# Performance work log

Hardware: AMD Instinct MI355X
Metric: run time of the kernel (lower is better)

The kernel has to match this reference:

```python
import jax, jax.numpy as jnp
import numpy as np

N_USERS, N_ITEMS, D, B = 16384, 4096, 64, 2048
NAN_FRAC = 0.7
EPS = 1e-8


def setup_inputs() -> dict:
    key = jax.random.key(0)
    k1, k2, k3, k4, k5 = jax.random.split(key, 5)
    ratings = jax.random.uniform(k1, (N_USERS, N_ITEMS), jnp.float32, 1.0, 5.0)
    miss = jax.random.uniform(k2, (N_USERS, N_ITEMS)) < NAN_FRAC
    rating_matrix = jnp.where(miss, jnp.nan, ratings)
    user_embeddings = jax.random.normal(k3, (N_USERS, D), jnp.float32)
    user_indices = jax.random.randint(k4, (B,), 0, N_USERS)
    item_indices = jax.random.randint(k5, (B,), 0, N_ITEMS)
    return {
        "rating_matrix": rating_matrix,
        "user_embeddings": user_embeddings,
        "user_indices": user_indices,
        "item_indices": item_indices,
    }


def reference(rating_matrix, user_embeddings, user_indices, item_indices):
    n_users = rating_matrix.shape[0]

    # per-user average over non-NaN ratings (0.0 if user has no ratings)
    valid_r = ~jnp.isnan(rating_matrix)                      # [N, I]
    r0 = jnp.where(valid_r, rating_matrix, 0.0)
    cnt = valid_r.sum(axis=1)
    avg_ratings = jnp.where(cnt > 0, r0.sum(axis=1) / jnp.maximum(cnt, 1), 0.0)  # [N]

    u = user_embeddings[user_indices]                        # [B, d]
    # cosine similarity of each query user vs all users
    dots = jnp.einsum('bd,nd->bn', u, user_embeddings)       # [B, N]
    mag_u = jnp.linalg.norm(u, axis=1, keepdims=True)        # [B, 1]
    mag_v = jnp.linalg.norm(user_embeddings, axis=1)[None]   # [1, N]
    sim = dots / (mag_u * mag_v + EPS)                       # [B, N]

    # ratings of all users on each query item
    ratings_col = rating_matrix[:, item_indices].T           # [B, N]
    mask = ~jnp.isnan(ratings_col)                           # valid neighbor ratings
    mask = mask & (jnp.arange(n_users)[None, :] != user_indices[:, None])  # exclude self

    diff = jnp.where(mask, ratings_col - avg_ratings[None, :], 0.0)
    sim_m = jnp.where(mask, sim, 0.0)
    num = (diff * sim_m).sum(axis=1)                         # [B]
    den = jnp.abs(sim_m).sum(axis=1)                         # [B]
    den_safe = jnp.where(den == 0, 1.0, den)

    avg_u = avg_ratings[user_indices]
    return jnp.where(den == 0, avg_u, avg_u + num / den_safe)
```

## Files before the change

kernel.cpp:

```cpp
#include <hip/hip_runtime.h>
#include <math.h>

#define NU   16384
#define NI   4096
#define DDIM 64
#define BB   2048

typedef unsigned short ushort_t;
typedef __attribute__((ext_vector_type(8))) short short8;
typedef __attribute__((ext_vector_type(4))) float f32x4;

static __device__ __forceinline__ unsigned short f2bf(float f) {
    union { float f; unsigned int u; } v; v.f = f;
    unsigned int u = v.u + 0x7FFFu + ((v.u >> 16) & 1u);
    return (unsigned short)(u >> 16);
}
static __device__ __forceinline__ float bf2f(unsigned short h) {
    union { unsigned int u; float f; } v; v.u = ((unsigned int)h) << 16;
    return v.f;
}

__global__ __launch_bounds__(256) void k_qprep(
    const float* __restrict__ E, const int* __restrict__ uidx,
    ushort_t* __restrict__ Ubf, int2* __restrict__ qinfo)
{
    const int lane = threadIdx.x & 63;
    const int b = blockIdx.x * 4 + (threadIdx.x >> 6);
    const int ub = uidx[b];
    const float e = E[(size_t)ub * DDIM + lane];
    float ss = e * e;
#pragma unroll
    for (int o = 32; o > 0; o >>= 1) ss += __shfl_xor(ss, o);
    Ubf[b * DDIM + lane] = f2bf(e);
    if (lane == 0) qinfo[b] = make_int2(ub, __float_as_int(rsqrtf(ss)));
}

__global__ __launch_bounds__(256) void k_rowgather(
    const float* __restrict__ R, const float* __restrict__ E,
    const int* __restrict__ iidx,
    float2* __restrict__ ani, ushort_t* __restrict__ Gbf)
{
    __shared__ ushort_t rowb[4][NI];
    __shared__ ushort_t s_ii[BB];
    const int tid  = threadIdx.x;
    const int lane = tid & 63;
    const int wid  = tid >> 6;

    for (int t = tid; t < BB; t += 256) s_ii[t] = (ushort_t)iidx[t];
    __syncthreads();

    const int gw = blockIdx.x * 4 + wid;
#pragma unroll 1
    for (int rr = 0; rr < 4; ++rr) {
        const int n = gw * 4 + rr;
        const float4* R4 = (const float4*)(R + (size_t)n * NI);
        float sum = 0.f, cnt = 0.f;
#pragma unroll
        for (int g = 0; g < 4; ++g) {
            float4 vv[4];
#pragma unroll
            for (int j = 0; j < 4; ++j) vv[j] = R4[(g * 4 + j) * 64 + lane];
#pragma unroll
            for (int j = 0; j < 4; ++j) {
                const float4 v = vv[j];
                if (v.x == v.x) { sum += v.x; cnt += 1.f; }
                if (v.y == v.y) { sum += v.y; cnt += 1.f; }
                if (v.z == v.z) { sum += v.z; cnt += 1.f; }
                if (v.w == v.w) { sum += v.w; cnt += 1.f; }
                ushort4 h;
                h.x = f2bf(v.x); h.y = f2bf(v.y); h.z = f2bf(v.z); h.w = f2bf(v.w);
                *(ushort4*)&rowb[wid][((g * 4 + j) * 64 + lane) * 4] = h;
            }
        }
        const float e = E[(size_t)n * DDIM + lane];
        float ss = e * e;
#pragma unroll
        for (int o = 32; o > 0; o >>= 1) ss += __shfl_xor(ss, o);
#pragma unroll
        for (int o = 32; o > 0; o >>= 1) {
            sum += __shfl_xor(sum, o);
            cnt += __shfl_xor(cnt, o);
        }
        if (lane == 0) {
            const float avg = (cnt > 0.f) ? (sum / cnt) : 0.f;
            ani[n] = make_float2(avg, rsqrtf(ss));
        }
        asm volatile("s_waitcnt lgkmcnt(0)" ::: "memory");
        ushort_t* Gn = Gbf + (size_t)n * BB;
#pragma unroll
        for (int it = 0; it < 32; ++it) {
            const int b = it * 64 + lane;
            Gn[b] = rowb[wid][s_ii[b]];
        }
    }
}

__global__ __launch_bounds__(256) void k_accum(
    const float* __restrict__ E, const ushort_t* __restrict__ Ubf,
    const ushort_t* __restrict__ Gbf, const float2* __restrict__ ani,
    const int2* __restrict__ qinfo, float2* __restrict__ partials)
{
    const int tid  = threadIdx.x;
    const int lane = tid & 63;
    const int w    = tid >> 6;
    const int lo   = lane & 15;
    const int hi   = lane >> 4;
    const int n0   = blockIdx.x * 16;

    short8 a[2];
#pragma unroll
    for (int kg = 0; kg < 2; ++kg) {
        const float* ep = E + (size_t)(n0 + lo) * DDIM + kg * 32 + hi * 8;
        const float4 e0 = *(const float4*)(ep);
        const float4 e1 = *(const float4*)(ep + 4);
        union { short8 v; ushort_t u[8]; } t;
        t.u[0] = f2bf(e0.x); t.u[1] = f2bf(e0.y); t.u[2] = f2bf(e0.z); t.u[3] = f2bf(e0.w);
        t.u[4] = f2bf(e1.x); t.u[5] = f2bf(e1.y); t.u[6] = f2bf(e1.z); t.u[7] = f2bf(e1.w);
        a[kg] = t.v;
    }
    float2 anir[4];
#pragma unroll
    for (int r = 0; r < 4; ++r) anir[r] = ani[n0 + hi * 4 + r];

    float2* pout = partials + (size_t)blockIdx.x * BB;

#pragma unroll 1
    for (int j = 0; j < 32; ++j) {
        const int b0 = (j * 4 + w) * 16;
        const int2 q = qinfo[b0 + lo];
        const float inv_mu = __int_as_float(q.y);

        short8 bf[2];
#pragma unroll
        for (int kg = 0; kg < 2; ++kg)
            bf[kg] = *(const short8*)(Ubf + (size_t)(b0 + lo) * DDIM + kg * 32 + hi * 8);

        f32x4 c = {0.f, 0.f, 0.f, 0.f};
        c = __builtin_amdgcn_mfma_f32_16x16x32_bf16(a[0], bf[0], c, 0, 0, 0);
        c = __builtin_amdgcn_mfma_f32_16x16x32_bf16(a[1], bf[1], c, 0, 0, 0);

        float fnum = 0.f, fden = 0.f;
#pragma unroll
        for (int r = 0; r < 4; ++r) {
            const int nr = n0 + hi * 4 + r;
            const float g = bf2f(Gbf[(size_t)nr * BB + b0 + lo]);
            const bool valid = (g == g) && (nr != q.x);
            const float s  = valid ? c[r] * (inv_mu * anir[r].y) : 0.f;
            const float gv = valid ? g : 0.f;
            fnum += (gv - anir[r].x) * s;
            fden += fabsf(s);
        }
        fnum += __shfl_xor(fnum, 16); fden += __shfl_xor(fden, 16);
        fnum += __shfl_xor(fnum, 32); fden += __shfl_xor(fden, 32);
        if (lane < 16) pout[b0 + lane] = make_float2(fnum, fden);
    }
}

__global__ __launch_bounds__(256) void k_final(
    const float2* __restrict__ partials, const float2* __restrict__ ani,
    const int2* __restrict__ qinfo, float* __restrict__ out)
{
    __shared__ float sn[8][32], sd[8][32];
    const int tid = threadIdx.x;
    const int bl  = tid & 31;
    const int ch  = tid >> 5;
    const int b   = blockIdx.x * 32 + bl;
    float n = 0.f, d = 0.f;
    for (int blk = ch; blk < NU / 16; blk += 8) {
        const float2 p = partials[(size_t)blk * BB + b];
        n += p.x; d += p.y;
    }
    sn[ch][bl] = n; sd[ch][bl] = d;
    __syncthreads();
    if (tid < 32) {
        float N = 0.f, D = 0.f;
#pragma unroll
        for (int c2 = 0; c2 < 8; ++c2) { N += sn[c2][tid]; D += sd[c2][tid]; }
        const int bb = blockIdx.x * 32 + tid;
        const float au = ani[qinfo[bb].x].x;
        out[bb] = (D == 0.f) ? au : (au + N / D);
    }
}

extern "C" void kernel_launch(void* const* d_in, const int* in_sizes, int n_in,
                              void* d_out, int out_size, void* d_ws, size_t ws_size,
                              hipStream_t stream)
{
    const float* R    = (const float*)d_in[0];
    const float* E    = (const float*)d_in[1];
    const int*   uidx = (const int*)d_in[2];
    const int*   iidx = (const int*)d_in[3];
    float* out = (float*)d_out;

    char* p = (char*)d_ws;
    ushort_t* Gbf   = (ushort_t*)p;              p += (size_t)NU * BB * 2;
    float2*   parts = (float2*)p;                p += (size_t)(NU / 16) * BB * 8;
    ushort_t* Ubf   = (ushort_t*)p;              p += (size_t)BB * DDIM * 2;
    float2*   ani   = (float2*)p;                p += (size_t)NU * 8;
    int2*     qinfo = (int2*)p;                  p += (size_t)BB * 8;

    k_qprep<<<BB / 4, 256, 0, stream>>>(E, uidx, Ubf, qinfo);
    k_rowgather<<<NU / 16, 256, 0, stream>>>(R, E, iidx, ani, Gbf);
    k_accum<<<NU / 16, 256, 0, stream>>>(E, Ubf, Gbf, ani, qinfo, parts);
    k_final<<<BB / 32, 256, 0, stream>>>(parts, ani, qinfo, out);
}
```

Baseline: 463.2 us.

## Fuse row gather and accumulation to keep gathered ratings in shared memory

Merges the row-gather and accumulate kernels into one block-per-16-users kernel. Each block gathers the selected item columns for its 16 users into a padded shared tile instead of writing a 64 MB bf16 gather buffer to global memory and reading it back. This removes that global round-trip and one launch. In exchange, shared memory per block rises to about 74 KB, which lowers occupancy, and the row-loading loop now has two block barriers per row.

Measured after the change: 440.5 us. 1.05x faster.

```diff
diff --git a/kernel.cpp b/kernel.cpp
--- a/kernel.cpp
+++ b/kernel.cpp
@@ -5,24 +5,25 @@
 #define NI   4096
 #define DDIM 64
 #define BB   2048
-
-typedef unsigned short ushort_t;
+#define GSTR 2052
+
+typedef unsigned short u16;
 typedef __attribute__((ext_vector_type(8))) short short8;
 typedef __attribute__((ext_vector_type(4))) float f32x4;
 
-static __device__ __forceinline__ unsigned short f2bf(float f) {
+static __device__ __forceinline__ u16 f2bf(float f) {
     union { float f; unsigned int u; } v; v.f = f;
     unsigned int u = v.u + 0x7FFFu + ((v.u >> 16) & 1u);
-    return (unsigned short)(u >> 16);
-}
-static __device__ __forceinline__ float bf2f(unsigned short h) {
+    return (u16)(u >> 16);
+}
+static __device__ __forceinline__ float bf2f(u16 h) {
     union { unsigned int u; float f; } v; v.u = ((unsigned int)h) << 16;
     return v.f;
 }
 
 __global__ __launch_bounds__(256) void k_qprep(
     const float* __restrict__ E, const int* __restrict__ uidx,
-    ushort_t* __restrict__ Ubf, int2* __restrict__ qinfo)
+    u16* __restrict__ Ubf, int2* __restrict__ qinfo)
 {
     const int lane = threadIdx.x & 63;
     const int b = blockIdx.x * 4 + (threadIdx.x >> 6);
@@ -35,77 +36,82 @@
     if (lane == 0) qinfo[b] = make_int2(ub, __float_as_int(rsqrtf(ss)));
 }
 
-__global__ __launch_bounds__(256) void k_rowgather(
+__global__ __launch_bounds__(256) void k_fused(
     const float* __restrict__ R, const float* __restrict__ E,
-    const int* __restrict__ iidx,
-    float2* __restrict__ ani, ushort_t* __restrict__ Gbf)
-{
-    __shared__ ushort_t rowb[4][NI];
-    __shared__ ushort_t s_ii[BB];
+    const int* __restrict__ iidx, const u16* __restrict__ Ubf,
+    const int2* __restrict__ qinfo, float2* __restrict__ partials,
+    float* __restrict__ avgAll)
+{
+    __shared__ u16 s_ii[BB];
+    __shared__ u16 row[NI];
+    __shared__ u16 g[16][GSTR];
+    __shared__ float sAvg[16], sInv[16];
+    __shared__ float redS[4], redC[4];
+
     const int tid  = threadIdx.x;
     const int lane = tid & 63;
     const int wid  = tid >> 6;
-
-    for (int t = tid; t < BB; t += 256) s_ii[t] = (ushort_t)iidx[t];
-    __syncthreads();
-
-    const int gw = blockIdx.x * 4 + wid;
-#pragma unroll 1
-    for (int rr = 0; rr < 4; ++rr) {
-        const int n = gw * 4 + rr;
-        const float4* R4 = (const float4*)(R + (size_t)n * NI);
-        float sum = 0.f, cnt = 0.f;
-#pragma unroll
-        for (int g = 0; g < 4; ++g) {
-            float4 vv[4];
-#pragma unroll
-            for (int j = 0; j < 4; ++j) vv[j] = R4[(g * 4 + j) * 64 + lane];
-#pragma unroll
-            for (int j = 0; j < 4; ++j) {
-                const float4 v = vv[j];
-                if (v.x == v.x) { sum += v.x; cnt += 1.f; }
-                if (v.y == v.y) { sum += v.y; cnt += 1.f; }
-                if (v.z == v.z) { sum += v.z; cnt += 1.f; }
-                if (v.w == v.w) { sum += v.w; cnt += 1.f; }
-                ushort4 h;
-                h.x = f2bf(v.x); h.y = f2bf(v.y); h.z = f2bf(v.z); h.w = f2bf(v.w);
-                *(ushort4*)&rowb[wid][((g * 4 + j) * 64 + lane) * 4] = h;
-            }
-        }
+    const int n0   = blockIdx.x * 16;
+
+    for (int t = tid; t < BB; t += 256) s_ii[t] = (u16)iidx[t];
+
+#pragma unroll
+    for (int rs = 0; rs < 4; ++rs) {
+        const int n = n0 + wid * 4 + rs;
         const float e = E[(size_t)n * DDIM + lane];
         float ss = e * e;
 #pragma unroll
         for (int o = 32; o > 0; o >>= 1) ss += __shfl_xor(ss, o);
+        if (lane == 0) sInv[wid * 4 + rs] = rsqrtf(ss);
+    }
+
+#pragma unroll 1
+    for (int rr = 0; rr < 16; ++rr) {
+        const int n = n0 + rr;
+        const float4* R4 = (const float4*)(R + (size_t)n * NI);
+        float4 vv[4];
+#pragma unroll
+        for (int j = 0; j < 4; ++j) vv[j] = R4[tid + j * 256];
+
+        __syncthreads();
+
+        float sum = 0.f, cnt = 0.f;
+#pragma unroll
+        for (int j = 0; j < 4; ++j) {
+            const float4 v = vv[j];
+            if (v.x == v.x) { sum += v.x; cnt += 1.f; }
+            if (v.y == v.y) { sum += v.y; cnt += 1.f; }
+            if (v.z == v.z) { sum += v.z; cnt += 1.f; }
+            if (v.w == v.w) { sum += v.w; cnt += 1.f; }
+            ushort4 h;
+            h.x = f2bf(v.x); h.y = f2bf(v.y); h.z = f2bf(v.z); h.w = f2bf(v.w);
+            *(ushort4*)&row[(tid + j * 256) * 4] = h;
+        }
 #pragma unroll
         for (int o = 32; o > 0; o >>= 1) {
             sum += __shfl_xor(sum, o);
             cnt += __shfl_xor(cnt, o);
         }
-        if (lane == 0) {
-            const float avg = (cnt > 0.f) ? (sum / cnt) : 0.f;
-            ani[n] = make_float2(avg, rsqrtf(ss));
-        }
-        asm volatile("s_waitcnt lgkmcnt(0)" ::: "memory");
-        ushort_t* Gn = Gbf + (size_t)n * BB;
-#pragma unroll
-        for (int it = 0; it < 32; ++it) {
-            const int b = it * 64 + lane;
-            Gn[b] = rowb[wid][s_ii[b]];
-        }
-    }
-}
-
-__global__ __launch_bounds__(256) void k_accum(
-    const float* __restrict__ E, const ushort_t* __restrict__ Ubf,
-    const ushort_t* __restrict__ Gbf, const float2* __restrict__ ani,
-    const int2* __restrict__ qinfo, float2* __restrict__ partials)
-{
-    const int tid  = threadIdx.x;
-    const int lane = tid & 63;
-    const int w    = tid >> 6;
-    const int lo   = lane & 15;
-    const int hi   = lane >> 4;
-    const int n0   = blockIdx.x * 16;
+        if (lane == 0) { redS[wid] = sum; redC[wid] = cnt; }
+
+        __syncthreads();
+        if (tid == 0) {
+            const float S = redS[0] + redS[1] + redS[2] + redS[3];
+            const float C = redC[0] + redC[1] + redC[2] + redC[3];
+            const float a = (C > 0.f) ? (S / C) : 0.f;
+            sAvg[rr] = a;
+            avgAll[n] = a;
+        }
+#pragma unroll
+        for (int t = 0; t < 8; ++t) {
+            const int b = tid + t * 256;
+            g[rr][b] = row[s_ii[b]];
+        }
+    }
+    __syncthreads();
+
+    const int lo = lane & 15;
+    const int hi = lane >> 4;
 
     short8 a[2];
 #pragma unroll
@@ -113,41 +119,39 @@
         const float* ep = E + (size_t)(n0 + lo) * DDIM + kg * 32 + hi * 8;
         const float4 e0 = *(const float4*)(ep);
         const float4 e1 = *(const float4*)(ep + 4);
-        union { short8 v; ushort_t u[8]; } t;
+        union { short8 v; u16 u[8]; } t;
         t.u[0] = f2bf(e0.x); t.u[1] = f2bf(e0.y); t.u[2] = f2bf(e0.z); t.u[3] = f2bf(e0.w);
         t.u[4] = f2bf(e1.x); t.u[5] = f2bf(e1.y); t.u[6] = f2bf(e1.z); t.u[7] = f2bf(e1.w);
         a[kg] = t.v;
     }
-    float2 anir[4];
-#pragma unroll
-    for (int r = 0; r < 4; ++r) anir[r] = ani[n0 + hi * 4 + r];
+    float avr[4], ivr[4];
+#pragma unroll
+    for (int r = 0; r < 4; ++r) { avr[r] = sAvg[hi * 4 + r]; ivr[r] = sInv[hi * 4 + r]; }
 
     float2* pout = partials + (size_t)blockIdx.x * BB;
 
 #pragma unroll 1
     for (int j = 0; j < 32; ++j) {
-        const int b0 = (j * 4 + w) * 16;
+        const int b0 = (j * 4 + wid) * 16;
         const int2 q = qinfo[b0 + lo];
         const float inv_mu = __int_as_float(q.y);
 
-        short8 bf[2];
-#pragma unroll
-        for (int kg = 0; kg < 2; ++kg)
-            bf[kg] = *(const short8*)(Ubf + (size_t)(b0 + lo) * DDIM + kg * 32 + hi * 8);
+        const short8 bf0 = *(const short8*)(Ubf + (size_t)(b0 + lo) * DDIM + hi * 8);
+        const short8 bf1 = *(const short8*)(Ubf + (size_t)(b0 + lo) * DDIM + 32 + hi * 8);
 
         f32x4 c = {0.f, 0.f, 0.f, 0.f};
-        c = __builtin_amdgcn_mfma_f32_16x16x32_bf16(a[0], bf[0], c, 0, 0, 0);
-        c = __builtin_amdgcn_mfma_f32_16x16x32_bf16(a[1], bf[1], c, 0, 0, 0);
+        c = __builtin_amdgcn_mfma_f32_16x16x32_bf16(a[0], bf0, c, 0, 0, 0);
+        c = __builtin_amdgcn_mfma_f32_16x16x32_bf16(a[1], bf1, c, 0, 0, 0);
 
         float fnum = 0.f, fden = 0.f;
 #pragma unroll
         for (int r = 0; r < 4; ++r) {
             const int nr = n0 + hi * 4 + r;
-            const float g = bf2f(Gbf[(size_t)nr * BB + b0 + lo]);
-            const bool valid = (g == g) && (nr != q.x);
-            const float s  = valid ? c[r] * (inv_mu * anir[r].y) : 0.f;
-            const float gv = valid ? g : 0.f;
-            fnum += (gv - anir[r].x) * s;
+            const float gg = bf2f(g[hi * 4 + r][b0 + lo]);
+            const bool valid = (gg == gg) && (nr != q.x);
+            const float s  = valid ? c[r] * (inv_mu * ivr[r]) : 0.f;
+            const float gv = valid ? gg : 0.f;
+            fnum += (gv - avr[r]) * s;
             fden += fabsf(s);
         }
         fnum += __shfl_xor(fnum, 16); fden += __shfl_xor(fden, 16);
@@ -157,8 +161,8 @@
 }
 
 __global__ __launch_bounds__(256) void k_final(
-    const float2* __restrict__ partials, const float2* __restrict__ ani,
-    const int2* __restrict__ qinfo, float* __restrict__ out)
+    const float2* __restrict__ partials, const int2* __restrict__ qinfo,
+    const float* __restrict__ avgAll, float* __restrict__ out)
 {
     __shared__ float sn[8][32], sd[8][32];
     const int tid = threadIdx.x;
@@ -177,7 +181,7 @@
 #pragma unroll
         for (int c2 = 0; c2 < 8; ++c2) { N += sn[c2][tid]; D += sd[c2][tid]; }
         const int bb = blockIdx.x * 32 + tid;
-        const float au = ani[qinfo[bb].x].x;
+        const float au = avgAll[qinfo[bb].x];
         out[bb] = (D == 0.f) ? au : (au + N / D);
     }
 }
@@ -193,14 +197,12 @@
     float* out = (float*)d_out;
 
     char* p = (char*)d_ws;
-    ushort_t* Gbf   = (ushort_t*)p;              p += (size_t)NU * BB * 2;
-    float2*   parts = (float2*)p;                p += (size_t)(NU / 16) * BB * 8;
-    ushort_t* Ubf   = (ushort_t*)p;              p += (size_t)BB * DDIM * 2;
-    float2*   ani   = (float2*)p;                p += (size_t)NU * 8;
-    int2*     qinfo = (int2*)p;                  p += (size_t)BB * 8;
+    float2* parts  = (float2*)p;  p += (size_t)(NU / 16) * BB * 8;
+    u16*    Ubf    = (u16*)p;     p += (size_t)BB * DDIM * 2;
+    int2*   qinfo  = (int2*)p;    p += (size_t)BB * 8;
+    float*  avgAll = (float*)p;   p += (size_t)NU * 4;
 
     k_qprep<<<BB / 4, 256, 0, stream>>>(E, uidx, Ubf, qinfo);
-    k_rowgather<<<NU / 16, 256, 0, stream>>>(R, E, iidx, ani, Gbf);
-    k_accum<<<NU / 16, 256, 0, stream>>>(E, Ubf, Gbf, ani, qinfo, parts);
-    k_final<<<BB / 32, 256, 0, stream>>>(parts, ani, qinfo, out);
-}
+    k_fused<<<NU / 16, 256, 0, stream>>>(R, E, iidx, Ubf, qinfo, parts, avgAll);
+    k_final<<<BB / 32, 256, 0, stream>>>(parts, qinfo, avgAll, out);
+}
```
